# Kernel tuning notes

Measured on AMD Instinct MI355X. Metric: run time of the kernel, lower is better.

## Reference

```python
import jax, jax.numpy as jnp
import numpy as np
from jax import lax

B, T, DW, H, NTYPES, DMAX = 256, 128, 300, 128, 8, 12
NLEV = DMAX + 1  # static number of bottom-up levels (tree depth capped at DMAX)


def _make_trees():
    """Random dependency trees: parent[b,i] < i, depth capped at DMAX.
    parent = -1 marks the single top node (child of ROOT) per sentence.
    height[b,i] = distance to farthest leaf (leaves have height 0)."""
    rng = np.random.RandomState(0)
    parent = -np.ones((B, T), np.int32)
    depth = np.zeros((B, T), np.int32)
    height = np.zeros((B, T), np.int32)
    for b in range(B):
        for i in range(1, T):
            p = rng.randint(0, i)
            if depth[b, p] >= DMAX:
                p = 0
            parent[b, i] = p
            depth[b, i] = depth[b, p] + 1
        for i in range(T - 1, 0, -1):
            p = parent[b, i]
            height[b, p] = max(height[b, p], height[b, i] + 1)
    dep_type = rng.randint(0, NTYPES, size=(B, T)).astype(np.int32)
    return parent, dep_type, height


def setup_inputs() -> dict:
    key = jax.random.key(0)
    k0, k1, k2, k3 = jax.random.split(key, 4)
    parent, dep_type, height = _make_trees()
    U = lambda k, s: jax.random.uniform(k, s, jnp.float32, -0.05, 0.05)  # keras 'uniform' init
    return {
        "token_emb": jax.random.normal(k0, (B, T, DW), jnp.float32),
        "W_wh": U(k1, (H, DW)),
        "b_wh": jnp.zeros((H,), jnp.float32),
        "W_hr": U(k2, (H, H)),
        "W_rel": U(k3, (NTYPES, H, H)),
        "parent": jnp.asarray(parent),
        "dep_type": jnp.asarray(dep_type),
        "height": jnp.asarray(height),
    }


def reference(token_emb, W_wh, b_wh, W_hr, W_rel, parent, dep_type, height):
    N = B * T
    x = token_emb.reshape(N, DW)
    par = parent.reshape(N)
    types = dep_type.reshape(N)
    hts = height.reshape(N)

    valid = par >= 0                      # edge child->parent exists
    base = (jnp.arange(N) // T) * T
    parg = jnp.where(valid, base + par, jnp.arange(N))  # global parent idx (self for top node)

    wx = x @ W_wh.T                       # [N,H]  focusRole / focusLinearPart (no bias)
    simple = jnp.tanh(wx + b_wh)          # [N,H]  focusHiddenSimple

    n_children = jnp.zeros((N,), jnp.float32).at[parg].add(valid.astype(jnp.float32))
    is_leaf = n_children == 0

    wx_par = wx[parg]                     # parent focusRole gathered per edge

    def step(h, k):
        # relation for every (child->parent) edge; children at lower heights are final
        rel = jnp.tanh(h @ W_hr.T + wx_par)            # [N,H]
        infl = jnp.zeros((N, H), h.dtype)
        for t in range(NTYPES):                         # small fixed relation-type loop
            m = (types == t) & valid
            infl = infl + jnp.where(m[:, None], rel @ W_rel[t].T, 0.0)
        seg = jnp.zeros((N, H), h.dtype).at[parg].add(infl)  # sumDependentInfluence
        cand = jnp.where(is_leaf[:, None], simple, jnp.tanh(seg + simple))
        h = jnp.where((hts == k)[:, None], cand, h)
        return h, None

    h0 = jnp.zeros((N, H), jnp.float32)
    h, _ = lax.scan(step, h0, jnp.arange(NLEV))
    return h.reshape(B, T, H)
```

## Files before the change

### kernel.cpp

```cpp
#include <hip/hip_runtime.h>
#include <math.h>

#define NB 256
#define NT 128
#define NDW 300
#define NH 128
#define NTYPE 8
#define NLEVEL 13
#define NN (NB*NT)

typedef __attribute__((ext_vector_type(8))) short short8;
typedef __attribute__((ext_vector_type(4))) float f32x4;

__device__ __forceinline__ unsigned int pack_bf16(float a, float b) {
  unsigned int ua = __float_as_uint(a); ua += 0x7fff + ((ua >> 16) & 1);
  unsigned int ub = __float_as_uint(b); ub += 0x7fff + ((ub >> 16) & 1);
  return (ua >> 16) | (ub & 0xffff0000u);
}

__device__ __forceinline__ float ftanh(float x) {
  float e = __expf(2.0f * x);
  return 1.0f - 2.0f * __builtin_amdgcn_rcpf(e + 1.0f);
}

__global__ __launch_bounds__(256) void wcvt_kernel(const float* __restrict__ Whr,
    const float* __restrict__ Wrel, uint2* __restrict__ bwT) {
  int flat = blockIdx.x*256 + threadIdx.x;
  int mat = flat >> 12, rem = flat & 4095;
  int d4 = rem >> 7, row = rem & 127;
  const float* src = (mat == 0) ? &Whr[row*NH + d4*4]
                                : &Wrel[(size_t)(mat-1)*NH*NH + row*NH + d4*4];
  float4 v = *(const float4*)src;
  uint2 u; u.x = pack_bf16(v.x, v.y); u.y = pack_bf16(v.z, v.w);
  bwT[flat] = u;
}

__global__ __launch_bounds__(256) void wx_kernel(const float* __restrict__ x,
    const float* __restrict__ Wwh, float* __restrict__ wx) {
  __shared__ __align__(16) unsigned int sA[64*16];
  __shared__ __align__(16) unsigned int sB[128*16];
  int tid = threadIdx.x;
  int wave = tid >> 6, lane = tid & 63;
  size_t rowbase = (size_t)blockIdx.x * 64;
  f32x4 acc[8];
  #pragma unroll
  for (int ni = 0; ni < 8; ni++) acc[ni] = (f32x4){0.f,0.f,0.f,0.f};
  for (int kc = 0; kc < 320; kc += 32) {
    __syncthreads();
    #pragma unroll
    for (int q = 0; q < 2; q++) {
      int flat = tid + q*256; int r = flat >> 3, f4 = flat & 7;
      int k0 = kc + f4*4;
      float4 v = make_float4(0.f,0.f,0.f,0.f);
      if (k0 + 3 < NDW) v = *(const float4*)&x[(rowbase + r)*NDW + k0];
      uint2 u; u.x = pack_bf16(v.x, v.y); u.y = pack_bf16(v.z, v.w);
      *(uint2*)&sA[r*16 + f4*2] = u;
    }
    #pragma unroll
    for (int q = 0; q < 4; q++) {
      int flat = tid + q*256; int r = flat >> 3, f4 = flat & 7;
      int k0 = kc + f4*4;
      float4 v = make_float4(0.f,0.f,0.f,0.f);
      if (k0 + 3 < NDW) v = *(const float4*)&Wwh[(size_t)r*NDW + k0];
      uint2 u; u.x = pack_bf16(v.x, v.y); u.y = pack_bf16(v.z, v.w);
      *(uint2*)&sB[r*16 + f4*2] = u;
    }
    __syncthreads();
    short8 a = *(const short8*)&sA[(wave*16 + (lane & 15))*16 + (lane >> 4)*4];
    #pragma unroll
    for (int ni = 0; ni < 8; ni++) {
      short8 b = *(const short8*)&sB[(ni*16 + (lane & 15))*16 + (lane >> 4)*4];
      acc[ni] = __builtin_amdgcn_mfma_f32_16x16x32_bf16(a, b, acc[ni], 0, 0, 0);
    }
  }
  int rbase = wave*16 + (lane >> 4)*4;
  #pragma unroll
  for (int ni = 0; ni < 8; ni++)
    #pragma unroll
    for (int reg = 0; reg < 4; reg++)
      wx[(rowbase + rbase + reg)*NH + ni*16 + (lane & 15)] = acc[ni][reg];
}

__device__ __forceinline__ void matvec4_T2(const uint2* __restrict__ wt,
    int lane, const float (*sv)[NH], float* o0, float* o1) {
  #pragma unroll
  for (int j = 0; j < 4; j++) { o0[j] = 0.f; o1[j] = 0.f; }
  #pragma unroll 4
  for (int d4 = 0; d4 < 32; d4++) {
    uint4 u = *(const uint4*)&wt[d4*128 + 2*lane];
    float w00 = __uint_as_float(u.x << 16), w01 = __uint_as_float(u.x & 0xffff0000u);
    float w02 = __uint_as_float(u.y << 16), w03 = __uint_as_float(u.y & 0xffff0000u);
    float w10 = __uint_as_float(u.z << 16), w11 = __uint_as_float(u.z & 0xffff0000u);
    float w12 = __uint_as_float(u.w << 16), w13 = __uint_as_float(u.w & 0xffff0000u);
    #pragma unroll
    for (int j = 0; j < 4; j++) {
      float4 v = *(const float4*)&sv[j][d4*4];
      o0[j] += w00*v.x + w01*v.y + w02*v.z + w03*v.w;
      o1[j] += w10*v.x + w11*v.y + w12*v.z + w13*v.w;
    }
  }
}

__device__ __forceinline__ void matvec4_mixed(const uint2* __restrict__ bwT,
    const int* tj, int lane, const float (*sv)[NH], float* o0, float* o1) {
  const uint2* wt0 = bwT + (size_t)(1 + tj[0])*4096;
  const uint2* wt1 = bwT + (size_t)(1 + tj[1])*4096;
  const uint2* wt2 = bwT + (size_t)(1 + tj[2])*4096;
  const uint2* wt3 = bwT + (size_t)(1 + tj[3])*4096;
  #pragma unroll
  for (int j = 0; j < 4; j++) { o0[j] = 0.f; o1[j] = 0.f; }
  #pragma unroll 2
  for (int d4 = 0; d4 < 32; d4++) {
    int off = d4*128 + 2*lane;
    uint4 u0 = *(const uint4*)&wt0[off];
    uint4 u1 = *(const uint4*)&wt1[off];
    uint4 u2 = *(const uint4*)&wt2[off];
    uint4 u3 = *(const uint4*)&wt3[off];
    const uint4 uu[4] = {u0, u1, u2, u3};
    #pragma unroll
    for (int j = 0; j < 4; j++) {
      float4 v = *(const float4*)&sv[j][d4*4];
      float w00 = __uint_as_float(uu[j].x << 16), w01 = __uint_as_float(uu[j].x & 0xffff0000u);
      float w02 = __uint_as_float(uu[j].y << 16), w03 = __uint_as_float(uu[j].y & 0xffff0000u);
      float w10 = __uint_as_float(uu[j].z << 16), w11 = __uint_as_float(uu[j].z & 0xffff0000u);
      float w12 = __uint_as_float(uu[j].w << 16), w13 = __uint_as_float(uu[j].w & 0xffff0000u);
      o0[j] += w00*v.x + w01*v.y + w02*v.z + w03*v.w;
      o1[j] += w10*v.x + w11*v.y + w12*v.z + w13*v.w;
    }
  }
}

__global__ __launch_bounds__(1024) void tree_kernel(
    const uint2* __restrict__ bwT, const float* __restrict__ bwh,
    const float* __restrict__ wx, const int* __restrict__ parent,
    const int* __restrict__ dep_type, const int* __restrict__ height,
    float* __restrict__ hbuf) {
  __shared__ float sseg[NT][NH];
  __shared__ __align__(16) float sh[16][4][NH];
  __shared__ int sord[NT], par_l[NT], typ_l[NT];
  __shared__ int gs[105], fill[104], hist[104];
  int b = blockIdx.x, tid = threadIdx.x;
  int wave = tid >> 6, lane = tid & 63;
  int e0 = 2*lane;
  for (int idx = tid; idx < NT*NH/4; idx += 1024)
    ((float4*)sseg)[idx] = make_float4(0.f,0.f,0.f,0.f);
  if (tid < 104) hist[tid] = 0;
  __syncthreads();
  int mykey = 0;
  if (tid < NT) {
    int g = b*NT + tid;
    int ty = dep_type[g];
    typ_l[tid] = ty;
    mykey = height[g]*NTYPE + ty;
    par_l[tid] = parent[g];
    atomicAdd(&hist[mykey], 1);
  }
  __syncthreads();
  if (tid == 0) {
    int acc = 0;
    for (int u = 0; u < 104; u++) { gs[u] = acc; acc += hist[u]; }
    gs[104] = acc;
  }
  __syncthreads();
  if (tid < 104) fill[tid] = gs[tid];
  __syncthreads();
  if (tid < NT) {
    int pos = atomicAdd(&fill[mykey], 1);
    sord[pos] = tid;
  }
  const float* wxb = wx + (size_t)b*NT*NH;
  float* hb = hbuf + (size_t)b*NT*NH;
  float2 bv = *(const float2*)&bwh[e0];
  __syncthreads();
  for (int k = 0; k < NLEVEL; k++) {
    int ls = gs[k*NTYPE], le = gs[k*NTYPE + NTYPE];
    int nbat = (le - ls + 3) >> 2;
    for (int bi = wave; bi < nbat; bi += 16) {
      int base = ls + bi*4;
      int cnt = le - base; if (cnt > 4) cnt = 4;
      int nl[4], pl[4], tj[4];
      #pragma unroll
      for (int j = 0; j < 4; j++) {
        int it = base + j; if (it >= le) it = le - 1;
        nl[j] = sord[it];
        pl[j] = par_l[nl[j]];
        tj[j] = typ_l[nl[j]];
      }
      float2 wxv[4], pw[4], sg[4];
      #pragma unroll
      for (int j = 0; j < 4; j++)
        wxv[j] = *(const float2*)&wxb[(size_t)nl[j]*NH + e0];
      #pragma unroll
      for (int j = 0; j < 4; j++) {
        int p = pl[j] >= 0 ? pl[j] : nl[j];
        pw[j] = *(const float2*)&wxb[(size_t)p*NH + e0];
      }
      #pragma unroll
      for (int j = 0; j < 4; j++)
        sg[j] = *(const float2*)&sseg[nl[j]][e0];
      #pragma unroll
      for (int j = 0; j < 4; j++) {
        float s0 = ftanh(wxv[j].x + bv.x);
        float s1 = ftanh(wxv[j].y + bv.y);
        float h0, h1;
        if (k == 0) { h0 = s0; h1 = s1; }
        else { h0 = ftanh(sg[j].x + s0); h1 = ftanh(sg[j].y + s1); }
        if (j < cnt)
          *(float2*)&hb[(size_t)nl[j]*NH + e0] = make_float2(h0, h1);
        *(float2*)&sh[wave][j][e0] = make_float2(h0, h1);
      }
      float g0v[4], g1v[4];
      matvec4_T2(bwT, lane, sh[wave], g0v, g1v);
      #pragma unroll
      for (int j = 0; j < 4; j++) {
        float r0 = ftanh(g0v[j] + pw[j].x);
        float r1 = ftanh(g1v[j] + pw[j].y);
        *(float2*)&sh[wave][j][e0] = make_float2(r0, r1);
      }
      float o0[4], o1[4];
      if (tj[0] == tj[1] && tj[1] == tj[2] && tj[2] == tj[3])
        matvec4_T2(bwT + (size_t)(1 + tj[0])*4096, lane, sh[wave], o0, o1);
      else
        matvec4_mixed(bwT, tj, lane, sh[wave], o0, o1);
      #pragma unroll
      for (int j = 0; j < 4; j++) if (j < cnt && pl[j] >= 0) {
        atomicAdd(&sseg[pl[j]][e0],     o0[j]);
        atomicAdd(&sseg[pl[j]][e0 + 1], o1[j]);
      }
    }
    __syncthreads();
  }
}

extern "C" void kernel_launch(void* const* d_in, const int* in_sizes, int n_in,
                              void* d_out, int out_size, void* d_ws, size_t ws_size,
                              hipStream_t stream) {
  const float* token  = (const float*)d_in[0];
  const float* Wwh    = (const float*)d_in[1];
  const float* bwh    = (const float*)d_in[2];
  const float* Whr    = (const float*)d_in[3];
  const float* Wrel   = (const float*)d_in[4];
  const int*   parent = (const int*)d_in[5];
  const int*   dep    = (const int*)d_in[6];
  const int*   height = (const int*)d_in[7];

  float* hbuf = (float*)d_out;
  float* wx   = (float*)d_ws;
  uint2* bwT  = (uint2*)((char*)d_ws + 16777216);

  wcvt_kernel<<<144, 256, 0, stream>>>(Whr, Wrel, bwT);
  wx_kernel<<<NN/64, 256, 0, stream>>>(token, Wwh, wx);
  tree_kernel<<<NB, 1024, 0, stream>>>(bwT, bwh, wx, parent, dep, height, hbuf);
}
```

Measured before the change: 292.8 us.

## Use bf16 dot2 instructions for tree matvecs and stage W_hr in LDS

Hidden and relation vectors are now packed to bf16 pairs in shared memory, and the matvecs use v_dot2_f32_bf16 instead of unpacking weights and doing fp32 FMAs. This cuts ALU work and LDS traffic per matvec. W_hr (32KB of bf16) is also copied into shared memory once per block, and the unroll factors are raised. In exchange the activations are rounded to bf16 before each matvec, which loses accuracy, and the extra LDS use may lower occupancy.

```diff
diff --git a/kernel.cpp b/kernel.cpp
--- a/kernel.cpp
+++ b/kernel.cpp
@@ -21,6 +21,12 @@
 __device__ __forceinline__ float ftanh(float x) {
   float e = __expf(2.0f * x);
   return 1.0f - 2.0f * __builtin_amdgcn_rcpf(e + 1.0f);
+}
+
+__device__ __forceinline__ float dot2a(unsigned int w, unsigned int v, float acc) {
+  float r;
+  asm("v_dot2_f32_bf16 %0, %1, %2, %3" : "=v"(r) : "v"(w), "v"(v), "v"(acc));
+  return r;
 }
 
 __global__ __launch_bounds__(256) void wcvt_kernel(const float* __restrict__ Whr,
@@ -81,51 +87,47 @@
       wx[(rowbase + rbase + reg)*NH + ni*16 + (lane & 15)] = acc[ni][reg];
 }
 
-__device__ __forceinline__ void matvec4_T2(const uint2* __restrict__ wt,
-    int lane, const float (*sv)[NH], float* o0, float* o1) {
+__device__ __forceinline__ void matvec4_d2(const uint2* __restrict__ wt,
+    int lane, const unsigned int (*sv)[64], float* o0, float* o1) {
   #pragma unroll
   for (int j = 0; j < 4; j++) { o0[j] = 0.f; o1[j] = 0.f; }
-  #pragma unroll 4
+  #pragma unroll 8
   for (int d4 = 0; d4 < 32; d4++) {
     uint4 u = *(const uint4*)&wt[d4*128 + 2*lane];
-    float w00 = __uint_as_float(u.x << 16), w01 = __uint_as_float(u.x & 0xffff0000u);
-    float w02 = __uint_as_float(u.y << 16), w03 = __uint_as_float(u.y & 0xffff0000u);
-    float w10 = __uint_as_float(u.z << 16), w11 = __uint_as_float(u.z & 0xffff0000u);
-    float w12 = __uint_as_float(u.w << 16), w13 = __uint_as_float(u.w & 0xffff0000u);
     #pragma unroll
     for (int j = 0; j < 4; j++) {
-      float4 v = *(const float4*)&sv[j][d4*4];
-      o0[j] += w00*v.x + w01*v.y + w02*v.z + w03*v.w;
-      o1[j] += w10*v.x + w11*v.y + w12*v.z + w13*v.w;
-    }
-  }
-}
-
-__device__ __forceinline__ void matvec4_mixed(const uint2* __restrict__ bwT,
-    const int* tj, int lane, const float (*sv)[NH], float* o0, float* o1) {
+      uint2 vv = *(const uint2*)&sv[j][d4*2];
+      o0[j] = dot2a(u.x, vv.x, o0[j]);
+      o0[j] = dot2a(u.y, vv.y, o0[j]);
+      o1[j] = dot2a(u.z, vv.x, o1[j]);
+      o1[j] = dot2a(u.w, vv.y, o1[j]);
+    }
+  }
+}
+
+__device__ __forceinline__ void matvec4_d2mixed(const uint2* __restrict__ bwT,
+    const int* tj, int lane, const unsigned int (*sv)[64], float* o0, float* o1) {
   const uint2* wt0 = bwT + (size_t)(1 + tj[0])*4096;
   const uint2* wt1 = bwT + (size_t)(1 + tj[1])*4096;
   const uint2* wt2 = bwT + (size_t)(1 + tj[2])*4096;
   const uint2* wt3 = bwT + (size_t)(1 + tj[3])*4096;
   #pragma unroll
   for (int j = 0; j < 4; j++) { o0[j] = 0.f; o1[j] = 0.f; }
-  #pragma unroll 2
+  #pragma unroll 4
   for (int d4 = 0; d4 < 32; d4++) {
     int off = d4*128 + 2*lane;
-    uint4 u0 = *(const uint4*)&wt0[off];
-    uint4 u1 = *(const uint4*)&wt1[off];
-    uint4 u2 = *(const uint4*)&wt2[off];
-    uint4 u3 = *(const uint4*)&wt3[off];
-    const uint4 uu[4] = {u0, u1, u2, u3};
+    uint4 uu[4];
+    uu[0] = *(const uint4*)&wt0[off];
+    uu[1] = *(const uint4*)&wt1[off];
+    uu[2] = *(const uint4*)&wt2[off];
+    uu[3] = *(const uint4*)&wt3[off];
     #pragma unroll
     for (int j = 0; j < 4; j++) {
-      float4 v = *(const float4*)&sv[j][d4*4];
-      float w00 = __uint_as_float(uu[j].x << 16), w01 = __uint_as_float(uu[j].x & 0xffff0000u);
-      float w02 = __uint_as_float(uu[j].y << 16), w03 = __uint_as_float(uu[j].y & 0xffff0000u);
-      float w10 = __uint_as_float(uu[j].z << 16), w11 = __uint_as_float(uu[j].z & 0xffff0000u);
-      float w12 = __uint_as_float(uu[j].w << 16), w13 = __uint_as_float(uu[j].w & 0xffff0000u);
-      o0[j] += w00*v.x + w01*v.y + w02*v.z + w03*v.w;
-      o1[j] += w10*v.x + w11*v.y + w12*v.z + w13*v.w;
+      uint2 vv = *(const uint2*)&sv[j][d4*2];
+      o0[j] = dot2a(uu[j].x, vv.x, o0[j]);
+      o0[j] = dot2a(uu[j].y, vv.y, o0[j]);
+      o1[j] = dot2a(uu[j].z, vv.x, o1[j]);
+      o1[j] = dot2a(uu[j].w, vv.y, o1[j]);
     }
   }
 }
@@ -136,7 +138,8 @@
     const int* __restrict__ dep_type, const int* __restrict__ height,
     float* __restrict__ hbuf) {
   __shared__ float sseg[NT][NH];
-  __shared__ __align__(16) float sh[16][4][NH];
+  __shared__ __align__(16) unsigned int ssh[16][4][64];
+  __shared__ __align__(16) uint2 sWhr[4096];
   __shared__ int sord[NT], par_l[NT], typ_l[NT];
   __shared__ int gs[105], fill[104], hist[104];
   int b = blockIdx.x, tid = threadIdx.x;
@@ -144,6 +147,8 @@
   int e0 = 2*lane;
   for (int idx = tid; idx < NT*NH/4; idx += 1024)
     ((float4*)sseg)[idx] = make_float4(0.f,0.f,0.f,0.f);
+  for (int idx = tid; idx < 4096; idx += 1024)
+    sWhr[idx] = bwT[idx];
   if (tid < 104) hist[tid] = 0;
   __syncthreads();
   int mykey = 0;
@@ -207,21 +212,22 @@
         else { h0 = ftanh(sg[j].x + s0); h1 = ftanh(sg[j].y + s1); }
         if (j < cnt)
           *(float2*)&hb[(size_t)nl[j]*NH + e0] = make_float2(h0, h1);
-        *(float2*)&sh[wave][j][e0] = make_float2(h0, h1);
+        ssh[wave][j][lane] = pack_bf16(h0, h1);
       }
       float g0v[4], g1v[4];
-      matvec4_T2(bwT, lane, sh[wave], g0v, g1v);
+      matvec4_d2(sWhr, lane, ssh[wave], g0v, g1v);
       #pragma unroll
       for (int j = 0; j < 4; j++) {
         float r0 = ftanh(g0v[j] + pw[j].x);
         float r1 = ftanh(g1v[j] + pw[j].y);
-        *(float2*)&sh[wave][j][e0] = make_float2(r0, r1);
+        ssh[wave][j][lane] = pack_bf16(r0, r1);
       }
       float o0[4], o1[4];
-      if (tj[0] == tj[1] && tj[1] == tj[2] && tj[2] == tj[3])
-        matvec4_T2(bwT + (size_t)(1 + tj[0])*4096, lane, sh[wave], o0, o1);
+      bool pure = (tj[0] == tj[1]) & (tj[1] == tj[2]) & (tj[2] == tj[3]);
+      if (pure)
+        matvec4_d2(bwT + (size_t)(1 + tj[0])*4096, lane, ssh[wave], o0, o1);
       else
-        matvec4_mixed(bwT, tj, lane, sh[wave], o0, o1);
+        matvec4_d2mixed(bwT, tj, lane, ssh[wave], o0, o1);
       #pragma unroll
       for (int j = 0; j < 4; j++) if (j < cnt && pl[j] >= 0) {
         atomicAdd(&sseg[pl[j]][e0],     o0[j]);
```

New measurement: 239.6 us. 1.22x faster.
